# Kernel tuning notes

Measured on AMD Instinct MI355X. Metric: run time of the kernel, lower is better.

The kernel has to match this reference:

```python
import jax, jax.numpy as jnp
import numpy as np

B, N, D = 1, 4301, 768          # batch, tokens (4200 patch + 1 cls + 100 det), dim
H, HD = 12, 64                  # heads, head_dim (all_head_dim = 768)
NDET = 100                      # det tokens at the end of the sequence
EPS = 1e-5                      # torch LayerNorm default eps
SCALE = HD ** -0.5


def setup_inputs() -> dict:
    key = jax.random.key(0)
    ks = jax.random.split(key, 10)
    w = lambda k: jax.random.normal(k, (D, D), dtype=jnp.float32) * 0.02
    return {
        "x": jax.random.normal(ks[0], (B, N, D), dtype=jnp.float32),
        "wq_p": w(ks[1]), "wk_p": w(ks[2]), "wv_p": w(ks[3]),
        "wq_d": w(ks[4]), "wk_d": w(ks[5]), "wv_d": w(ks[6]),
        "bq_p": jnp.zeros((D,), jnp.float32), "bv_p": jnp.zeros((D,), jnp.float32),
        "bq_d": jnp.zeros((D,), jnp.float32), "bv_d": jnp.zeros((D,), jnp.float32),
        "ln_g": jnp.ones((D,), jnp.float32), "ln_b": jnp.zeros((D,), jnp.float32),
        "wo_p": w(ks[7]), "bo_p": jnp.zeros((D,), jnp.float32),
        "wo_d": w(ks[8]), "bo_d": jnp.zeros((D,), jnp.float32),
    }


def reference(x, wq_p, wk_p, wv_p, wq_d, wk_d, wv_d,
              bq_p, bv_p, bq_d, bv_d, ln_g, ln_b,
              wo_p, bo_p, wo_d, bo_d):
    xp = x[:, :-NDET, :]                       # [B, N-100, D] patch (+cls) tokens
    xd = x[:, -NDET:, :]                       # [B, 100, D]   det tokens
    # separate patch/det QKV projections (subln=True path; k has no bias)
    q = jnp.concatenate([xp @ wq_p.T + bq_p, xd @ wq_d.T + bq_d], axis=1)
    k = jnp.concatenate([xp @ wk_p.T,        xd @ wk_d.T],        axis=1)
    v = jnp.concatenate([xp @ wv_p.T + bv_p, xd @ wv_d.T + bv_d], axis=1)
    split = lambda t: t.reshape(B, N, H, HD).transpose(0, 2, 1, 3)  # [B,H,N,HD]
    q, k, v = split(q) * SCALE, split(k), split(v)
    # unfused attention (memory_efficient_attention_pytorch, attn_mask=None)
    attn = jax.nn.softmax(jnp.einsum("bhqd,bhkd->bhqk", q, k), axis=-1)
    o = jnp.einsum("bhqk,bhkd->bhqd", attn, v)
    o = o.transpose(0, 2, 1, 3).reshape(B, N, D)
    # inner_attn_ln (LayerNorm over all_head_dim)
    mu = o.mean(-1, keepdims=True)
    var = ((o - mu) ** 2).mean(-1, keepdims=True)
    o = (o - mu) * jax.lax.rsqrt(var + EPS) * ln_g + ln_b
    # separate patch/det output projections
    out = jnp.concatenate([o[:, :-NDET, :] @ wo_p.T + bo_p,
                           o[:, -NDET:, :] @ wo_d.T + bo_d], axis=1)
    return out
```

## Files before the change

kernel.cpp:

```cpp
#include <hip/hip_runtime.h>
#include <hip/hip_bf16.h>

#define NT 4301
#define NP 4201
#define NDET 100
#define DMODEL 768
#define NHEAD 12
#define HD 64
#define LN_EPS 1e-5f
#define LOG2E 1.4426950408889634f
#define QSCALE (0.125f * LOG2E)
#define NTP 4352
#define NCHUNK 68
#define FRAGSZ 512
#define CHUNKSZ 4096

typedef __hip_bfloat16 bf16;
typedef __attribute__((ext_vector_type(4))) float f32x4;
typedef __attribute__((ext_vector_type(8))) short frag8;

__device__ __forceinline__ unsigned short fast_bf16(float x) {
    unsigned int u = __float_as_uint(x);
    u += 0x7FFFu + ((u >> 16) & 1u);
    return (unsigned short)(u >> 16);
}

__global__ __launch_bounds__(256) void cast_all_kernel(
    const float* __restrict__ x,
    const float* __restrict__ w0, const float* __restrict__ w1,
    const float* __restrict__ w2, const float* __restrict__ w3,
    const float* __restrict__ w4, const float* __restrict__ w5,
    const float* __restrict__ w6, const float* __restrict__ w7,
    bf16* __restrict__ dst, int nx, int nw, int total) {
    int i4 = (blockIdx.x * 256 + threadIdx.x) * 4;
    if (i4 >= total) return;
    const float* s;
    int off;
    if (i4 < nx) {
        s = x; off = i4;
    } else {
        int r = i4 - nx;
        int w = r / nw;
        off = r - w * nw;
        s = w0;
        if (w == 1) s = w1; else if (w == 2) s = w2; else if (w == 3) s = w3;
        else if (w == 4) s = w4; else if (w == 5) s = w5;
        else if (w == 6) s = w6; else if (w == 7) s = w7;
    }
    float4 v = *(const float4*)(s + off);
    bf16 o[4] = {__float2bfloat16(v.x), __float2bfloat16(v.y),
                 __float2bfloat16(v.z), __float2bfloat16(v.w)};
    *(ushort4*)(dst + i4) = *(ushort4*)o;
}

__global__ __launch_bounds__(256, 4) void qkv_kernel(
    const bf16* __restrict__ xb, const bf16* __restrict__ wbase,
    const float* __restrict__ bq_p, const float* __restrict__ bq_d,
    const float* __restrict__ bv_p, const float* __restrict__ bv_d,
    bf16* __restrict__ Qb, bf16* __restrict__ Ksw, bf16* __restrict__ Vsw) {
    __shared__ bf16 As[64][32];
    __shared__ bf16 Bs[192][32];

    const int tid = threadIdx.x;
    const int wave = tid >> 6, lane = tid & 63;
    const int quad = lane >> 4, l16 = lane & 15;
    const int bx = blockIdx.x;
    const int h = blockIdx.y;
    const int is_det = bx >= 66;
    const int row0 = is_det ? NP + (bx - 66) * 64 : bx * 64;
    const int Mlim = is_det ? NT : NP;
    const int col0 = h * 64;
    const size_t nw = (size_t)DMODEL * DMODEL;
    const bf16* W = wbase + (is_det ? 3 * nw : 0);

    const f32x4 z4 = {0.f, 0.f, 0.f, 0.f};
    f32x4 acc[4][3];
#pragma unroll
    for (int r4 = 0; r4 < 4; ++r4)
#pragma unroll
        for (int f = 0; f < 3; ++f) acc[r4][f] = z4;

    const int srow = tid >> 2;
    const int scol8 = (tid & 3) * 8;
    int a_r = row0 + srow;
    if (a_r >= Mlim) a_r = Mlim - 1;
    const bf16* ap = xb + (size_t)a_r * DMODEL + scol8;
    const bf16* bp = W + (size_t)(col0 + srow) * DMODEL + scol8;

    uint4 areg  = *(const uint4*)(ap);
    uint4 breg0 = *(const uint4*)(bp);
    uint4 breg1 = *(const uint4*)(bp + nw);
    uint4 breg2 = *(const uint4*)(bp + 2 * nw);

    for (int k0 = 0; k0 < DMODEL; k0 += 32) {
        __syncthreads();
        *(uint4*)(&As[srow][scol8]) = areg;
        *(uint4*)(&Bs[srow][scol8]) = breg0;
        *(uint4*)(&Bs[64 + srow][scol8]) = breg1;
        *(uint4*)(&Bs[128 + srow][scol8]) = breg2;
        if (k0 + 32 < DMODEL) {
            areg  = *(const uint4*)(ap + k0 + 32);
            breg0 = *(const uint4*)(bp + k0 + 32);
            breg1 = *(const uint4*)(bp + nw + k0 + 32);
            breg2 = *(const uint4*)(bp + 2 * nw + k0 + 32);
        }
        __asm__ volatile("s_waitcnt lgkmcnt(0)" ::: "memory");
        __builtin_amdgcn_s_barrier();
        __asm__ volatile("" ::: "memory");
        frag8 af[4], bfr[3];
#pragma unroll
        for (int r4 = 0; r4 < 4; ++r4)
            af[r4] = *(const frag8*)(&As[r4 * 16 + l16][quad * 8]);
#pragma unroll
        for (int f = 0; f < 3; ++f)
            bfr[f] = *(const frag8*)(&Bs[wave * 48 + f * 16 + l16][quad * 8]);
#pragma unroll
        for (int r4 = 0; r4 < 4; ++r4)
#pragma unroll
            for (int f = 0; f < 3; ++f)
                acc[r4][f] = __builtin_amdgcn_mfma_f32_16x16x32_bf16(af[r4], bfr[f], acc[r4][f], 0, 0, 0);
        __asm__ volatile("" ::: "memory");
    }

#pragma unroll
    for (int f = 0; f < 3; ++f) {
        const int oc = 3 * wave + f;
        const int opi = oc >> 2;
        const int cin = (oc & 3) * 16 + l16;
        const int c = col0 + cin;
        float bv = 0.f, scale = 1.f;
        if (opi == 0) { bv = (is_det ? bq_d : bq_p)[c]; scale = QSCALE; }
        else if (opi == 2) { bv = (is_det ? bv_d : bv_p)[c]; }
#pragma unroll
        for (int r4 = 0; r4 < 4; ++r4) {
#pragma unroll
            for (int j = 0; j < 4; ++j) {
                const int r = row0 + r4 * 16 + quad * 4 + j;
                if (r >= Mlim) continue;
                const bf16 val = __float2bfloat16((acc[r4][f][j] + bv) * scale);
                if (opi == 0) {
                    Qb[(size_t)r * DMODEL + c] = val;
                } else if (opi == 1) {
                    const int cc = r >> 6, tf = (r >> 4) & 3, ln = r & 15;
                    const int s = cin >> 5, qd = (cin >> 3) & 3, je = cin & 7;
                    Ksw[((size_t)(h * NCHUNK + cc) * 8 + tf * 2 + s) * FRAGSZ +
                        (qd * 16 + ln) * 8 + je] = val;
                } else {
                    const int t = cin >> 4, le = cin & 15;
                    const int cc = r >> 6, rr = r & 63;
                    const int sv = rr >> 5, qv = (rr >> 3) & 3, je = rr & 7;
                    Vsw[((size_t)(h * NCHUNK + cc) * 8 + t * 2 + sv) * FRAGSZ +
                        (qv * 16 + le) * 8 + je] = val;
                }
            }
        }
    }
}

__global__ __launch_bounds__(256, 2) void attn_kernel(
    const bf16* __restrict__ Q, const bf16* __restrict__ Ksw,
    const bf16* __restrict__ Vsw, float* __restrict__ O_part,
    float* __restrict__ l_part, int cpb) {
    __shared__ unsigned short Ps[4][32][72];

    const int tid = threadIdx.x;
    const int wave = tid >> 6, lane = tid & 63;
    const int quad = lane >> 4, l16 = lane & 15;
    const int h = blockIdx.y;
    const int z = blockIdx.z;
    const int qbase = blockIdx.x * 128;
    const int hoff = h * HD;
    const int c0 = z * cpb, c1 = c0 + cpb;

    frag8 ones;
#pragma unroll
    for (int j = 0; j < 8; ++j) ones[j] = (short)0x3F80;

    frag8 qf[2][2];
#pragma unroll
    for (int g = 0; g < 2; ++g) {
        int qr = qbase + wave * 32 + g * 16 + l16;
        if (qr >= NT) qr = NT - 1;
#pragma unroll
        for (int s = 0; s < 2; ++s)
            qf[g][s] = *(const frag8*)(Q + (size_t)qr * DMODEL + hoff + s * 32 + quad * 8);
    }

    const bf16* kb0 = Ksw + (size_t)h * NCHUNK * CHUNKSZ + lane * 8;
    const bf16* vb0 = Vsw + (size_t)h * NCHUNK * CHUNKSZ + lane * 8;

    const f32x4 z4 = {0.f, 0.f, 0.f, 0.f};
    f32x4 accO[2][4], accL[2];
#pragma unroll
    for (int g = 0; g < 2; ++g) {
        accL[g] = z4;
#pragma unroll
        for (int t = 0; t < 4; ++t) accO[g][t] = z4;
    }

    for (int c = c0; c < c1; ++c) {
        const bf16* kc = kb0 + (size_t)c * CHUNKSZ;
        const bf16* vc = vb0 + (size_t)c * CHUNKSZ;
        frag8 kf[8], vf[8];
#pragma unroll
        for (int f = 0; f < 8; ++f) {
            kf[f] = *(const frag8*)(kc + f * FRAGSZ);
            vf[f] = *(const frag8*)(vc + f * FRAGSZ);
        }

        f32x4 S[2][4];
#pragma unroll
        for (int g = 0; g < 2; ++g)
#pragma unroll
            for (int t = 0; t < 4; ++t) {
                f32x4 s0 = __builtin_amdgcn_mfma_f32_16x16x32_bf16(qf[g][0], kf[t * 2 + 0], z4, 0, 0, 0);
                S[g][t]  = __builtin_amdgcn_mfma_f32_16x16x32_bf16(qf[g][1], kf[t * 2 + 1], s0, 0, 0, 0);
            }
        if (c == NCHUNK - 1) {
            const int kbase = c * 64;
#pragma unroll
            for (int t = 0; t < 4; ++t)
                if (kbase + t * 16 + l16 >= NT)
#pragma unroll
                    for (int g = 0; g < 2; ++g)
                        S[g][t][0] = S[g][t][1] = S[g][t][2] = S[g][t][3] = -1e30f;
        }
#pragma unroll
        for (int g = 0; g < 2; ++g)
#pragma unroll
            for (int t = 0; t < 4; ++t)
#pragma unroll
                for (int j = 0; j < 4; ++j)
                    Ps[wave][g * 16 + quad * 4 + j][t * 16 + l16] =
                        fast_bf16(__builtin_exp2f(S[g][t][j]));
        __asm__ volatile("" ::: "memory");
#pragma unroll
        for (int s = 0; s < 2; ++s)
#pragma unroll
            for (int g = 0; g < 2; ++g) {
                frag8 pf = *(const frag8*)(&Ps[wave][g * 16 + l16][s * 32 + quad * 8]);
                accL[g] = __builtin_amdgcn_mfma_f32_16x16x32_bf16(pf, ones, accL[g], 0, 0, 0);
#pragma unroll
                for (int t = 0; t < 4; ++t)
                    accO[g][t] = __builtin_amdgcn_mfma_f32_16x16x32_bf16(pf, vf[t * 2 + s], accO[g][t], 0, 0, 0);
            }
        __asm__ volatile("" ::: "memory");
    }

    float* Op = O_part + (size_t)z * NT * DMODEL;
#pragma unroll
    for (int g = 0; g < 2; ++g)
#pragma unroll
        for (int j = 0; j < 4; ++j) {
            const int r = qbase + wave * 32 + g * 16 + quad * 4 + j;
            if (r < NT) {
#pragma unroll
                for (int t = 0; t < 4; ++t)
                    Op[(size_t)r * DMODEL + hoff + t * 16 + l16] = accO[g][t][j];
                if (l16 == 0)
                    l_part[((size_t)z * NHEAD + h) * NTP + r] = accL[g][j];
            }
        }
}

__global__ __launch_bounds__(256) void reduce_ln_kernel(
    const float* __restrict__ O_part, const float* __restrict__ l_part,
    const float* __restrict__ g, const float* __restrict__ b,
    bf16* __restrict__ out, int nsplit) {
    const int n = blockIdx.x;
    const int tid = threadIdx.x;
    float vals[3];
#pragma unroll
    for (int i = 0; i < 3; ++i) {
        const int d = tid + i * 256;
        const int hh = d >> 6;
        float o = 0.f, lv = 0.f;
        for (int s = 0; s < nsplit; ++s) {
            o  += O_part[((size_t)s * NT + n) * DMODEL + d];
            lv += l_part[((size_t)s * NHEAD + hh) * NTP + n];
        }
        vals[i] = o / lv;
    }
    float s = vals[0] + vals[1] + vals[2];
    float s2 = vals[0] * vals[0] + vals[1] * vals[1] + vals[2] * vals[2];
#pragma unroll
    for (int off = 1; off < 64; off <<= 1) {
        s += __shfl_xor(s, off);
        s2 += __shfl_xor(s2, off);
    }
    __shared__ float ss[4], ss2[4];
    const int wave = tid >> 6, lane = tid & 63;
    if (lane == 0) { ss[wave] = s; ss2[wave] = s2; }
    __syncthreads();
    s = ss[0] + ss[1] + ss[2] + ss[3];
    s2 = ss2[0] + ss2[1] + ss2[2] + ss2[3];
    const float mu = s * (1.0f / 768.0f);
    float var = s2 * (1.0f / 768.0f) - mu * mu;
    const float inv = rsqrtf(var + LN_EPS);
#pragma unroll
    for (int i = 0; i < 3; ++i) {
        const int d = tid + i * 256;
        const float v = (vals[i] - mu) * inv * g[d] + b[d];
        out[(size_t)n * DMODEL + d] = __float2bfloat16(v);
    }
}

__global__ __launch_bounds__(256) void out_kernel(
    const bf16* __restrict__ Lb, const bf16* __restrict__ wo,
    const float* __restrict__ bo_p, const float* __restrict__ bo_d,
    float* __restrict__ out) {
    __shared__ bf16 As[64][32];
    __shared__ bf16 Bs[64][32];

    const int tid = threadIdx.x;
    const int wave = tid >> 6, lane = tid & 63;
    const int quad = lane >> 4, l16 = lane & 15;
    const int bx = blockIdx.x;
    const int is_det = bx >= 66;
    const int row0 = is_det ? NP + (bx - 66) * 64 : bx * 64;
    const int Mlim = is_det ? NT : NP;
    const int col0 = blockIdx.y * 64;
    const size_t nw = (size_t)DMODEL * DMODEL;
    const bf16* B = wo + (is_det ? nw : 0);
    const float* bias = is_det ? bo_d : bo_p;

    f32x4 acc[4] = {{0.f,0.f,0.f,0.f},{0.f,0.f,0.f,0.f},{0.f,0.f,0.f,0.f},{0.f,0.f,0.f,0.f}};

    const int arow = tid >> 2;
    const int acol = (tid & 3) * 8;
    int a_r = row0 + arow;
    if (a_r >= Mlim) a_r = Mlim - 1;
    const bf16* ap = Lb + (size_t)a_r * DMODEL + acol;
    const bf16* bp = B + (size_t)(col0 + arow) * DMODEL + acol;

    uint4 areg = *(const uint4*)(ap);
    uint4 breg = *(const uint4*)(bp);

    for (int k0 = 0; k0 < DMODEL; k0 += 32) {
        __syncthreads();
        *(uint4*)(&As[arow][acol]) = areg;
        *(uint4*)(&Bs[arow][acol]) = breg;
        if (k0 + 32 < DMODEL) {
            areg = *(const uint4*)(ap + k0 + 32);
            breg = *(const uint4*)(bp + k0 + 32);
        }
        __asm__ volatile("s_waitcnt lgkmcnt(0)" ::: "memory");
        __builtin_amdgcn_s_barrier();
        __asm__ volatile("" ::: "memory");
        frag8 af = *(const frag8*)(&As[wave * 16 + l16][quad * 8]);
#pragma unroll
        for (int t = 0; t < 4; ++t) {
            frag8 bfq = *(const frag8*)(&Bs[t * 16 + l16][quad * 8]);
            acc[t] = __builtin_amdgcn_mfma_f32_16x16x32_bf16(af, bfq, acc[t], 0, 0, 0);
        }
        __asm__ volatile("" ::: "memory");
    }

    const int rbase = row0 + wave * 16 + quad * 4;
#pragma unroll
    for (int t = 0; t < 4; ++t) {
        const int c = col0 + t * 16 + l16;
        const float bv = bias[c];
#pragma unroll
        for (int j = 0; j < 4; ++j) {
            const int r = rbase + j;
            if (r < Mlim) out[(size_t)r * DMODEL + c] = acc[t][j] + bv;
        }
    }
}

extern "C" void kernel_launch(void* const* d_in, const int* in_sizes, int n_in,
                              void* d_out, int out_size, void* d_ws, size_t ws_size,
                              hipStream_t stream) {
    const float* x    = (const float*)d_in[0];
    const float* wq_p = (const float*)d_in[1];
    const float* wk_p = (const float*)d_in[2];
    const float* wv_p = (const float*)d_in[3];
    const float* wq_d = (const float*)d_in[4];
    const float* wk_d = (const float*)d_in[5];
    const float* wv_d = (const float*)d_in[6];
    const float* bq_p = (const float*)d_in[7];
    const float* bv_p = (const float*)d_in[8];
    const float* bq_d = (const float*)d_in[9];
    const float* bv_d = (const float*)d_in[10];
    const float* ln_g = (const float*)d_in[11];
    const float* ln_b = (const float*)d_in[12];
    const float* wo_p = (const float*)d_in[13];
    const float* bo_p = (const float*)d_in[14];
    const float* wo_d = (const float*)d_in[15];
    const float* bo_d = (const float*)d_in[16];
    float* out = (float*)d_out;

    const size_t nx  = (size_t)NT * DMODEL;
    const size_t nsw = (size_t)NHEAD * NCHUNK * CHUNKSZ;
    const size_t nw  = (size_t)DMODEL * DMODEL;

    char* ws = (char*)d_ws;
    bf16* xb   = (bf16*)ws; ws += nx * 2;
    bf16* wqkv = (bf16*)ws; ws += 6 * nw * 2;
    bf16* wob  = (bf16*)ws; ws += 2 * nw * 2;
    bf16* Qb   = (bf16*)ws; ws += nx * 2;
    bf16* Ksw  = (bf16*)ws; ws += nsw * 2;
    bf16* Vsw  = (bf16*)ws; ws += nsw * 2;
    const size_t fixed = (size_t)(ws - (char*)d_ws);

    const size_t per_split = nx * 4 + (size_t)NHEAD * NTP * 4;
    int nsplit = 1;
    if (ws_size >= fixed + 4 * per_split) nsplit = 4;
    else if (ws_size >= fixed + 2 * per_split) nsplit = 2;
    const int cpb = NCHUNK / nsplit;

    float* O_part = (float*)ws;
    float* l_part = (float*)(ws + (size_t)nsplit * nx * 4);
    bf16* Lb = xb;

    const int total = (int)(nx + 8 * nw);
    cast_all_kernel<<<dim3((total / 4 + 255) / 256), dim3(256), 0, stream>>>(
        x, wq_p, wk_p, wv_p, wq_d, wk_d, wv_d, wo_p, wo_d, xb, (int)nx, (int)nw, total);

    qkv_kernel<<<dim3(68, 12), dim3(256), 0, stream>>>(
        xb, wqkv, bq_p, bq_d, bv_p, bv_d, Qb, Ksw, Vsw);

    attn_kernel<<<dim3(34, NHEAD, nsplit), dim3(256), 0, stream>>>(
        Qb, Ksw, Vsw, O_part, l_part, cpb);

    reduce_ln_kernel<<<dim3(NT), dim3(256), 0, stream>>>(
        O_part, l_part, ln_g, ln_b, Lb, nsplit);

    out_kernel<<<dim3(68, 12), dim3(256), 0, stream>>>(Lb, wob, bo_p, bo_d, out);
}
```

Measured before the change: 277.0 us.

## Pack bf16 conversion in attention, vectorize reduce-LN, enlarge out-proj M tile

In the attention kernel, the hand-written bf16 rounding is replaced by a paired float2-to-bf162 intrinsic, so two probabilities convert at once. The reduce+LayerNorm kernel now uses 192 threads that each load float4 partials and store four packed bf16 values, replacing scalar accesses. The output projection grows its tile from 64 to 128 rows per block, giving each wave a 32-row slab so B-tile fetches are reused across two MFMA rows. The det tokens now go to a single block. The larger tile halves the grid size, which may reduce parallelism on a large GPU.

```diff
diff --git a/kernel.cpp b/kernel.cpp
--- a/kernel.cpp
+++ b/kernel.cpp
@@ -18,12 +18,6 @@
 typedef __hip_bfloat16 bf16;
 typedef __attribute__((ext_vector_type(4))) float f32x4;
 typedef __attribute__((ext_vector_type(8))) short frag8;
-
-__device__ __forceinline__ unsigned short fast_bf16(float x) {
-    unsigned int u = __float_as_uint(x);
-    u += 0x7FFFu + ((u >> 16) & 1u);
-    return (unsigned short)(u >> 16);
-}
 
 __global__ __launch_bounds__(256) void cast_all_kernel(
     const float* __restrict__ x,
@@ -230,9 +224,14 @@
 #pragma unroll
             for (int t = 0; t < 4; ++t)
 #pragma unroll
-                for (int j = 0; j < 4; ++j)
-                    Ps[wave][g * 16 + quad * 4 + j][t * 16 + l16] =
-                        fast_bf16(__builtin_exp2f(S[g][t][j]));
+                for (int j = 0; j < 4; j += 2) {
+                    float2 f2 = make_float2(__builtin_exp2f(S[g][t][j]),
+                                            __builtin_exp2f(S[g][t][j + 1]));
+                    __hip_bfloat162 b2 = __float22bfloat162_rn(f2);
+                    unsigned int u = *(unsigned int*)&b2;
+                    Ps[wave][g * 16 + quad * 4 + j][t * 16 + l16] = (unsigned short)u;
+                    Ps[wave][g * 16 + quad * 4 + j + 1][t * 16 + l16] = (unsigned short)(u >> 16);
+                }
         __asm__ volatile("" ::: "memory");
 #pragma unroll
         for (int s = 0; s < 2; ++s)
@@ -263,108 +262,132 @@
         }
 }
 
-__global__ __launch_bounds__(256) void reduce_ln_kernel(
+__global__ __launch_bounds__(192) void reduce_ln_kernel(
     const float* __restrict__ O_part, const float* __restrict__ l_part,
     const float* __restrict__ g, const float* __restrict__ b,
     bf16* __restrict__ out, int nsplit) {
     const int n = blockIdx.x;
     const int tid = threadIdx.x;
-    float vals[3];
-#pragma unroll
-    for (int i = 0; i < 3; ++i) {
-        const int d = tid + i * 256;
-        const int hh = d >> 6;
-        float o = 0.f, lv = 0.f;
-        for (int s = 0; s < nsplit; ++s) {
-            o  += O_part[((size_t)s * NT + n) * DMODEL + d];
-            lv += l_part[((size_t)s * NHEAD + hh) * NTP + n];
-        }
-        vals[i] = o / lv;
-    }
-    float s = vals[0] + vals[1] + vals[2];
-    float s2 = vals[0] * vals[0] + vals[1] * vals[1] + vals[2] * vals[2];
+    const int d0 = tid * 4;
+    const int hh = d0 >> 6;
+
+    float4 o = make_float4(0.f, 0.f, 0.f, 0.f);
+    float lv = 0.f;
+    for (int s = 0; s < nsplit; ++s) {
+        float4 v = *(const float4*)(O_part + ((size_t)s * NT + n) * DMODEL + d0);
+        o.x += v.x; o.y += v.y; o.z += v.z; o.w += v.w;
+        lv += l_part[((size_t)s * NHEAD + hh) * NTP + n];
+    }
+    const float inv_l = 1.0f / lv;
+    float vals[4] = {o.x * inv_l, o.y * inv_l, o.z * inv_l, o.w * inv_l};
+
+    float s = vals[0] + vals[1] + vals[2] + vals[3];
+    float s2 = vals[0] * vals[0] + vals[1] * vals[1] + vals[2] * vals[2] + vals[3] * vals[3];
 #pragma unroll
     for (int off = 1; off < 64; off <<= 1) {
         s += __shfl_xor(s, off);
         s2 += __shfl_xor(s2, off);
     }
-    __shared__ float ss[4], ss2[4];
+    __shared__ float ss[3], ss2[3];
     const int wave = tid >> 6, lane = tid & 63;
     if (lane == 0) { ss[wave] = s; ss2[wave] = s2; }
     __syncthreads();
-    s = ss[0] + ss[1] + ss[2] + ss[3];
-    s2 = ss2[0] + ss2[1] + ss2[2] + ss2[3];
+    s = ss[0] + ss[1] + ss[2];
+    s2 = ss2[0] + ss2[1] + ss2[2];
     const float mu = s * (1.0f / 768.0f);
     float var = s2 * (1.0f / 768.0f) - mu * mu;
     const float inv = rsqrtf(var + LN_EPS);
-#pragma unroll
-    for (int i = 0; i < 3; ++i) {
-        const int d = tid + i * 256;
+
+    unsigned short pk[4];
+#pragma unroll
+    for (int i = 0; i < 4; ++i) {
+        const int d = d0 + i;
         const float v = (vals[i] - mu) * inv * g[d] + b[d];
-        out[(size_t)n * DMODEL + d] = __float2bfloat16(v);
-    }
-}
-
-__global__ __launch_bounds__(256) void out_kernel(
+        bf16 bb = __float2bfloat16(v);
+        pk[i] = *(unsigned short*)&bb;
+    }
+    *(ushort4*)(out + (size_t)n * DMODEL + d0) = *(ushort4*)pk;
+}
+
+__global__ __launch_bounds__(256, 2) void out_kernel(
     const bf16* __restrict__ Lb, const bf16* __restrict__ wo,
     const float* __restrict__ bo_p, const float* __restrict__ bo_d,
     float* __restrict__ out) {
-    __shared__ bf16 As[64][32];
+    __shared__ bf16 As[128][32];
     __shared__ bf16 Bs[64][32];
 
     const int tid = threadIdx.x;
     const int wave = tid >> 6, lane = tid & 63;
     const int quad = lane >> 4, l16 = lane & 15;
     const int bx = blockIdx.x;
-    const int is_det = bx >= 66;
-    const int row0 = is_det ? NP + (bx - 66) * 64 : bx * 64;
+    const int is_det = bx >= 33;
+    const int row0 = is_det ? NP : bx * 128;
     const int Mlim = is_det ? NT : NP;
     const int col0 = blockIdx.y * 64;
     const size_t nw = (size_t)DMODEL * DMODEL;
     const bf16* B = wo + (is_det ? nw : 0);
     const float* bias = is_det ? bo_d : bo_p;
 
-    f32x4 acc[4] = {{0.f,0.f,0.f,0.f},{0.f,0.f,0.f,0.f},{0.f,0.f,0.f,0.f},{0.f,0.f,0.f,0.f}};
-
-    const int arow = tid >> 2;
-    const int acol = (tid & 3) * 8;
+    const f32x4 z4 = {0.f, 0.f, 0.f, 0.f};
+    f32x4 acc[2][4];
+#pragma unroll
+    for (int gg = 0; gg < 2; ++gg)
+#pragma unroll
+        for (int t = 0; t < 4; ++t) acc[gg][t] = z4;
+
+    const int arow = tid >> 1;
+    const int acol = (tid & 1) * 16;
     int a_r = row0 + arow;
     if (a_r >= Mlim) a_r = Mlim - 1;
     const bf16* ap = Lb + (size_t)a_r * DMODEL + acol;
-    const bf16* bp = B + (size_t)(col0 + arow) * DMODEL + acol;
-
-    uint4 areg = *(const uint4*)(ap);
-    uint4 breg = *(const uint4*)(bp);
+    const int brow = tid >> 2;
+    const int bcol = (tid & 3) * 8;
+    const bf16* bp = B + (size_t)(col0 + brow) * DMODEL + bcol;
+
+    uint4 areg0 = *(const uint4*)(ap);
+    uint4 areg1 = *(const uint4*)(ap + 8);
+    uint4 breg  = *(const uint4*)(bp);
 
     for (int k0 = 0; k0 < DMODEL; k0 += 32) {
         __syncthreads();
-        *(uint4*)(&As[arow][acol]) = areg;
-        *(uint4*)(&Bs[arow][acol]) = breg;
+        *(uint4*)(&As[arow][acol]) = areg0;
+        *(uint4*)(&As[arow][acol + 8]) = areg1;
+        *(uint4*)(&Bs[brow][bcol]) = breg;
         if (k0 + 32 < DMODEL) {
-            areg = *(const uint4*)(ap + k0 + 32);
-            breg = *(const uint4*)(bp + k0 + 32);
+            areg0 = *(const uint4*)(ap + k0 + 32);
+            areg1 = *(const uint4*)(ap + k0 + 40);
+            breg  = *(const uint4*)(bp + k0 + 32);
         }
         __asm__ volatile("s_waitcnt lgkmcnt(0)" ::: "memory");
         __builtin_amdgcn_s_barrier();
         __asm__ volatile("" ::: "memory");
-        frag8 af = *(const frag8*)(&As[wave * 16 + l16][quad * 8]);
+        frag8 af[2], bfq[4];
+#pragma unroll
+        for (int gg = 0; gg < 2; ++gg)
+            af[gg] = *(const frag8*)(&As[wave * 32 + gg * 16 + l16][quad * 8]);
+#pragma unroll
+        for (int t = 0; t < 4; ++t)
+            bfq[t] = *(const frag8*)(&Bs[t * 16 + l16][quad * 8]);
+#pragma unroll
+        for (int gg = 0; gg < 2; ++gg)
+#pragma unroll
+            for (int t = 0; t < 4; ++t)
+                acc[gg][t] = __builtin_amdgcn_mfma_f32_16x16x32_bf16(af[gg], bfq[t], acc[gg][t], 0, 0, 0);
+        __asm__ volatile("" ::: "memory");
+    }
+
+#pragma unroll
+    for (int gg = 0; gg < 2; ++gg) {
+        const int rbase = row0 + wave * 32 + gg * 16 + quad * 4;
 #pragma unroll
         for (int t = 0; t < 4; ++t) {
-            frag8 bfq = *(const frag8*)(&Bs[t * 16 + l16][quad * 8]);
-            acc[t] = __builtin_amdgcn_mfma_f32_16x16x32_bf16(af, bfq, acc[t], 0, 0, 0);
-        }
-        __asm__ volatile("" ::: "memory");
-    }
-
-    const int rbase = row0 + wave * 16 + quad * 4;
-#pragma unroll
-    for (int t = 0; t < 4; ++t) {
-        const int c = col0 + t * 16 + l16;
-        const float bv = bias[c];
-#pragma unroll
-        for (int j = 0; j < 4; ++j) {
-            const int r = rbase + j;
-            if (r < Mlim) out[(size_t)r * DMODEL + c] = acc[t][j] + bv;
+            const int c = col0 + t * 16 + l16;
+            const float bv = bias[c];
+#pragma unroll
+            for (int j = 0; j < 4; ++j) {
+                const int r = rbase + j;
+                if (r < Mlim) out[(size_t)r * DMODEL + c] = acc[gg][t][j] + bv;
+            }
         }
     }
 }
@@ -424,8 +447,8 @@
     attn_kernel<<<dim3(34, NHEAD, nsplit), dim3(256), 0, stream>>>(
         Qb, Ksw, Vsw, O_part, l_part, cpb);
 
-    reduce_ln_kernel<<<dim3(NT), dim3(256), 0, stream>>>(
+    reduce_ln_kernel<<<dim3(NT), dim3(192), 0, stream>>>(
         O_part, l_part, ln_g, ln_b, Lb, nsplit);
 
-    out_kernel<<<dim3(68, 12), dim3(256), 0, stream>>>(Lb, wob, bo_p, bo_d, out);
-}
+    out_kernel<<<dim3(34, 12), dim3(256), 0, stream>>>(Lb, wob, bo_p, bo_d, out);
+}
```

Result: faster. 264.9 us (-4.4%).
